# Optimization experiments

Hardware: AMD Instinct MI355X
Metric: run time of the kernel (lower is better)

Reference implementation:

```python
import jax, jax.numpy as jnp
import numpy as np

V, D, T, L, H = 32000, 1024, 2048, 2, 16
HS = D // H  # per-head dim (head_size // nheads)
FF = 4 * D
EPS = 1e-5


def _ln(x, g, b):
    m = jnp.mean(x, axis=-1, keepdims=True)
    v = jnp.mean((x - m) ** 2, axis=-1, keepdims=True)
    return (x - m) * jax.lax.rsqrt(v + EPS) * g + b


def setup_inputs() -> dict:
    key = jax.random.key(0)
    ks = jax.random.split(key, 16)
    s = lambda k, shape, fan: jax.random.normal(k, shape, jnp.float32) * (fan ** -0.5)
    return {
        "inputs": jax.random.randint(ks[0], (1, T), 0, V, dtype=jnp.int64),
        "tok_emb": s(ks[1], (V, D), D),
        "pos_emb": s(ks[2], (T, D), D),
        "ln1_g": jnp.ones((L, D)), "ln1_b": jnp.zeros((L, D)),
        "wq": s(ks[3], (L, H, D, HS), D),
        "wk": s(ks[4], (L, H, D, HS), D),
        "wv": s(ks[5], (L, H, D, HS), D),
        "ln2_g": jnp.ones((L, D)), "ln2_b": jnp.zeros((L, D)),
        "w1": s(ks[6], (L, D, FF), D), "b1": jnp.zeros((L, FF)),
        "w2": s(ks[7], (L, FF, D), FF), "b2": jnp.zeros((L, D)),
        "lnf_g": jnp.ones((D,)), "lnf_b": jnp.zeros((D,)),
        "w_un": s(ks[8], (D, V), D), "b_un": jnp.zeros((V,)),
    }


def reference(inputs, tok_emb, pos_emb, ln1_g, ln1_b, wq, wk, wv,
              ln2_g, ln2_b, w1, b1, w2, b2, lnf_g, lnf_b, w_un, b_un):
    b, t = inputs.shape
    x = tok_emb[inputs] + pos_emb[:t]  # [B,T,D]
    mask = jnp.tril(jnp.ones((t, t), dtype=bool))
    scale = jnp.asarray(D, x.dtype) ** -0.5  # source scales by x.shape[-1]**-0.5
    neg_inf = jnp.asarray(-jnp.inf, x.dtype)
    for l in range(L):
        h = _ln(x, ln1_g[l], ln1_b[l])
        q = jnp.einsum('btc,hcs->bhts', h, wq[l])
        k = jnp.einsum('btc,hcs->bhts', h, wk[l])
        v = jnp.einsum('btc,hcs->bhts', h, wv[l])
        scores = jnp.einsum('bhts,bhus->bhtu', q, k) * scale  # [B,H,T,T]
        scores = jnp.where(mask, scores, neg_inf)
        p = jax.nn.softmax(scores, axis=-1)
        att = jnp.einsum('bhtu,bhus->bhts', p, v)  # [B,H,T,HS]
        att = att.transpose(0, 2, 1, 3).reshape(b, t, H * HS)
        x = x + att
        h = _ln(x, ln2_g[l], ln2_b[l])
        h = jax.nn.relu(h @ w1[l] + b1[l]) @ w2[l] + b2[l]
        x = x + h
    x = _ln(x, lnf_g, lnf_b)
    return x @ w_un + b_un  # [B,T,V]
```

## Files before the change

kernel.cpp:

```cpp
#include <hip/hip_runtime.h>
#include <hip/hip_bf16.h>

#define TT 2048
#define DD 1024
#define NH 16
#define HSZ 64
#define FFD 4096
#define VV 32000
#define NL 2

typedef __bf16 bf16x8 __attribute__((ext_vector_type(8)));
typedef float f32x4 __attribute__((ext_vector_type(4)));

__device__ __forceinline__ unsigned short f2bf(float f) {
    unsigned int u = __float_as_uint(f);
    return (unsigned short)((u + 0x7FFFu + ((u >> 16) & 1u)) >> 16);
}

#define GLL(gsrc, ldst) \
  __builtin_amdgcn_global_load_lds((const __attribute__((address_space(1))) void*)(gsrc), \
                                   (__attribute__((address_space(3))) void*)(ldst), 16, 0, 0)

#define SWZ64(L)  ((L) ^ ((((L) >> 7) & 3) << 4))
#define SWZ128(L) ((L) ^ ((((L) >> 7) & 7) << 4))

#define VMW(n) asm volatile("s_waitcnt vmcnt(" #n ")" ::: "memory")

__global__ __launch_bounds__(256) void embed_kernel(
    const int* __restrict__ idx, const float* __restrict__ tok,
    const float* __restrict__ pos, float* __restrict__ x)
{
    int t = blockIdx.x;
    int d4 = threadIdx.x * 4;
    int token = idx[t];
    float4 a = *(const float4*)&tok[(size_t)token * DD + d4];
    float4 p = *(const float4*)&pos[(size_t)t * DD + d4];
    float4 r;
    r.x = a.x + p.x; r.y = a.y + p.y; r.z = a.z + p.z; r.w = a.w + p.w;
    *(float4*)&x[(size_t)t * DD + d4] = r;
}

__global__ __launch_bounds__(256) void ln_kernel(
    const float* __restrict__ x, const float* __restrict__ g,
    const float* __restrict__ b, unsigned short* __restrict__ out)
{
    int t = blockIdx.x;
    int tid = threadIdx.x;
    int d4 = tid * 4;
    float4 xv = *(const float4*)&x[(size_t)t * DD + d4];
    float s  = xv.x + xv.y + xv.z + xv.w;
    float s2 = xv.x*xv.x + xv.y*xv.y + xv.z*xv.z + xv.w*xv.w;
    #pragma unroll
    for (int off = 32; off >= 1; off >>= 1) {
        s  += __shfl_xor(s,  off);
        s2 += __shfl_xor(s2, off);
    }
    __shared__ float ls[4], ls2[4];
    int w = tid >> 6;
    if ((tid & 63) == 0) { ls[w] = s; ls2[w] = s2; }
    __syncthreads();
    float sum  = ls[0] + ls[1] + ls[2] + ls[3];
    float sum2 = ls2[0] + ls2[1] + ls2[2] + ls2[3];
    float mean = sum * (1.0f / DD);
    float var  = sum2 * (1.0f / DD) - mean * mean;
    float r = rsqrtf(var + 1e-5f);
    float4 gv = *(const float4*)&g[d4];
    float4 bv = *(const float4*)&b[d4];
    ushort4 pk;
    pk.x = f2bf((xv.x - mean) * r * gv.x + bv.x);
    pk.y = f2bf((xv.y - mean) * r * gv.y + bv.y);
    pk.z = f2bf((xv.z - mean) * r * gv.z + bv.z);
    pk.w = f2bf((xv.w - mean) * r * gv.w + bv.w);
    *(ushort4*)&out[(size_t)t * DD + d4] = pk;
}

__global__ __launch_bounds__(256) void tcast(
    const float* __restrict__ src, unsigned short* __restrict__ dst,
    int R, int C, size_t sstride, size_t dstride)
{
    __shared__ float tile[64][65];
    const float* s = src + (size_t)blockIdx.z * sstride;
    unsigned short* d = dst + (size_t)blockIdx.z * dstride;
    int c0 = blockIdx.x * 64, r0 = blockIdx.y * 64;
    #pragma unroll
    for (int i = 0; i < 16; ++i) {
        int id = i * 256 + threadIdx.x;
        int rr = id >> 6, cc = id & 63;
        tile[rr][cc] = s[(size_t)(r0 + rr) * C + (c0 + cc)];
    }
    __syncthreads();
    #pragma unroll
    for (int i = 0; i < 16; ++i) {
        int id = i * 256 + threadIdx.x;
        int cc = id >> 6, rr = id & 63;
        d[(size_t)(c0 + cc) * R + (r0 + rr)] = f2bf(tile[rr][cc]);
    }
}

__global__ __launch_bounds__(256) void qkv_tcast(
    const float* __restrict__ wq, const float* __restrict__ wk,
    const float* __restrict__ wv, unsigned short* __restrict__ dst)
{
    __shared__ float tile[64][65];
    int l = blockIdx.z;
    int mat = blockIdx.y >> 4, hh = blockIdx.y & 15;
    const float* s = (mat == 0) ? wq : (mat == 1) ? wk : wv;
    s += (((size_t)l * NH + hh) * DD) * HSZ;
    int r0 = blockIdx.x * 64;
    #pragma unroll
    for (int i = 0; i < 16; ++i) {
        int id = i * 256 + threadIdx.x;
        int rr = id >> 6, cc = id & 63;
        tile[rr][cc] = s[(size_t)(r0 + rr) * HSZ + cc];
    }
    __syncthreads();
    unsigned short* d = dst + (size_t)l * 3072 * DD + ((size_t)mat * DD + hh * HSZ) * DD;
    #pragma unroll
    for (int i = 0; i < 16; ++i) {
        int id = i * 256 + threadIdx.x;
        int cc = id >> 6, rr = id & 63;
        d[(size_t)cc * DD + (r0 + rr)] = f2bf(tile[rr][cc]);
    }
}

template<int EPI, int BN>
__global__ __launch_bounds__(256) void mgemm(
    const unsigned short* __restrict__ A, const unsigned short* __restrict__ Bt,
    const float* __restrict__ bias, void* __restrict__ outp,
    int M, int N, int K, int Kst)
{
    constexpr int FN = BN / 64 * 2;
    __shared__ unsigned short As[3][128 * 32];
    __shared__ unsigned short Bs[3][BN * 32];
    int tid = threadIdx.x;
    int w = tid >> 6, lane = tid & 63;
    int l15 = lane & 15, l4 = lane >> 4;
    int bm = blockIdx.y * 128, bn = blockIdx.x * BN;
    int wr = (w >> 1) * 64, wc = (w & 1) * (BN / 2);
    if (EPI == 3) {
        int z = blockIdx.z;
        A  += (size_t)z * K;
        Bt += (size_t)z * K;
        outp = (float*)outp + (size_t)z * TT * DD;
    }

    f32x4 zz = {0.f, 0.f, 0.f, 0.f};
    f32x4 acc[4][FN];
    #pragma unroll
    for (int m = 0; m < 4; ++m)
        #pragma unroll
        for (int n = 0; n < FN; ++n) acc[m][n] = zz;

    int t16 = tid * 16;
    int lg = SWZ64(t16);
    int srow = lg >> 6;
    int skel = (lg & 63) >> 1;
    const unsigned short* aS0 = A + (size_t)(bm + srow) * Kst + skel;
    const unsigned short* aS1 = A + (size_t)(bm + 64 + srow) * Kst + skel;
    const unsigned short* bS0 = Bt + (size_t)(bn + srow) * Kst + skel;
    const unsigned short* bS1 = Bt + (size_t)(bn + 64 + srow) * Kst + skel;

    #define STAGE(t, slot) do { int kk_ = (t) * 32; \
        GLL(aS0 + kk_, (char*)As[slot] + w * 1024); \
        GLL(aS1 + kk_, (char*)As[slot] + 4096 + w * 1024); \
        GLL(bS0 + kk_, (char*)Bs[slot] + w * 1024); \
        if (BN == 128) GLL(bS1 + kk_, (char*)Bs[slot] + 4096 + w * 1024); } while (0)

    int aoff[4], boff[FN];
    #pragma unroll
    for (int m = 0; m < 4; ++m)
        aoff[m] = SWZ64((wr + m * 16 + l15) * 64 + l4 * 16);
    #pragma unroll
    for (int n = 0; n < FN; ++n)
        boff[n] = SWZ64((wc + n * 16 + l15) * 64 + l4 * 16);

    int nt = K >> 5;
    STAGE(0, 0);
    STAGE(1, 1);
    STAGE(2, 2);
    int slot = 0;
    for (int t = 0; t < nt; ++t) {
        if (BN == 128) {
            if (t + 2 < nt)      VMW(8);
            else if (t + 1 < nt) VMW(4);
            else                 VMW(0);
        } else {
            if (t + 2 < nt)      VMW(6);
            else if (t + 1 < nt) VMW(3);
            else                 VMW(0);
        }
        __builtin_amdgcn_sched_barrier(0);
        __builtin_amdgcn_s_barrier();
        __builtin_amdgcn_sched_barrier(0);
        bf16x8 af[4], bfr[FN];
        #pragma unroll
        for (int m = 0; m < 4; ++m) af[m] = *(const bf16x8*)((const char*)As[slot] + aoff[m]);
        #pragma unroll
        for (int n = 0; n < FN; ++n) bfr[n] = *(const bf16x8*)((const char*)Bs[slot] + boff[n]);
        #pragma unroll
        for (int m = 0; m < 4; ++m)
            #pragma unroll
            for (int n = 0; n < FN; ++n)
                acc[m][n] = __builtin_amdgcn_mfma_f32_16x16x32_bf16(af[m], bfr[n], acc[m][n], 0, 0, 0);
        __builtin_amdgcn_sched_barrier(0);
        __builtin_amdgcn_s_barrier();
        __builtin_amdgcn_sched_barrier(0);
        if (t + 3 < nt) STAGE(t + 3, slot);
        slot = (slot == 2) ? 0 : slot + 1;
    }
    #undef STAGE

    #pragma unroll
    for (int m = 0; m < 4; ++m) {
        int row0 = bm + wr + m * 16 + l4 * 4;
        #pragma unroll
        for (int n = 0; n < FN; ++n) {
            int col = bn + wc + n * 16 + l15;
            f32x4 v = acc[m][n];
            if (EPI == 0) {
                int mat = col >> 10, hh = (col >> 6) & 15, ss = col & 63;
                unsigned short* base = (unsigned short*)outp + (size_t)mat * ((size_t)NH * TT * HSZ);
                if (mat < 2) {
                    #pragma unroll
                    for (int i = 0; i < 4; ++i)
                        base[((size_t)hh * TT + row0 + i) * HSZ + ss] = f2bf(v[i]);
                } else {
                    ushort4 pk;
                    pk.x = f2bf(v[0]); pk.y = f2bf(v[1]); pk.z = f2bf(v[2]); pk.w = f2bf(v[3]);
                    *(ushort4*)&base[((size_t)hh * HSZ + ss) * TT + row0] = pk;
                }
            } else if (EPI == 1) {
                float bb = bias[col];
                unsigned short* o = (unsigned short*)outp;
                #pragma unroll
                for (int i = 0; i < 4; ++i)
                    o[(size_t)(row0 + i) * FFD + col] = f2bf(fmaxf(v[i] + bb, 0.f));
            } else if (EPI == 2) {
                float bb = bias[col];
                float* xx = (float*)outp;
                #pragma unroll
                for (int i = 0; i < 4; ++i)
                    xx[(size_t)(row0 + i) * DD + col] += v[i] + bb;
            } else {
                float* xx = (float*)outp;
                #pragma unroll
                for (int i = 0; i < 4; ++i)
                    xx[(size_t)(row0 + i) * DD + col] = v[i];
            }
        }
    }
}

__global__ __launch_bounds__(256) void ffn2_reduce(
    const float* __restrict__ P, const float* __restrict__ b2,
    float* __restrict__ x)
{
    int t = blockIdx.x;
    int d4 = threadIdx.x * 4;
    size_t o = (size_t)t * DD + d4;
    float4 p0 = *(const float4*)&P[o];
    float4 p1 = *(const float4*)&P[o + (size_t)TT * DD];
    float4 bb = *(const float4*)&b2[d4];
    float4 xv = *(float4*)&x[o];
    xv.x += p0.x + p1.x + bb.x;
    xv.y += p0.y + p1.y + bb.y;
    xv.z += p0.z + p1.z + bb.z;
    xv.w += p0.w + p1.w + bb.w;
    *(float4*)&x[o] = xv;
}

__global__ __launch_bounds__(512, 2) void mgemm256(
    const unsigned short* __restrict__ A, const unsigned short* __restrict__ Bt,
    const float* __restrict__ bias, float* __restrict__ outp,
    int M, int N, int K)
{
    __shared__ unsigned short As[2][2][128 * 64];
    __shared__ unsigned short Bs[2][2][128 * 64];
    int tid = threadIdx.x;
    int w = tid >> 6, lane = tid & 63;
    int l15 = lane & 15, l4 = lane >> 4;
    int wr = w >> 2, wc = w & 3;
    int bid = blockIdx.x;
    int xcd = bid & 7, j = bid >> 3;
    int mt = j & 7, p = xcd * 16 + (j >> 3);
    if (p >= N / 256) return;
    int bm = mt * 256, bn = p * 256;

    f32x4 zz = {0.f, 0.f, 0.f, 0.f};
    f32x4 acc[8][4];
    #pragma unroll
    for (int m = 0; m < 8; ++m)
        #pragma unroll
        for (int n = 0; n < 4; ++n) acc[m][n] = zz;

    int L0 = w * 1024 + lane * 16;
    int Ls = SWZ128(L0);
    int srow = Ls >> 7;
    int skel = (Ls & 127) >> 1;
    const unsigned short* aS[2], *bS[2];
    aS[0] = A + (size_t)(bm + srow) * K + skel;
    aS[1] = A + (size_t)(bm + 128 + srow) * K + skel;
    bS[0] = Bt + (size_t)(bn + srow) * K + skel;
    bS[1] = Bt + (size_t)(bn + 128 + srow) * K + skel;
    size_t g1 = (size_t)64 * K;

    #define STAGE6(t, buf) do { int kk_ = (t) * 64; \
        GLL(aS[0] + kk_,      (char*)As[buf][0] + w * 1024); \
        GLL(aS[0] + g1 + kk_, (char*)As[buf][0] + 8192 + w * 1024); \
        GLL(aS[1] + kk_,      (char*)As[buf][1] + w * 1024); \
        GLL(aS[1] + g1 + kk_, (char*)As[buf][1] + 8192 + w * 1024); \
        GLL(bS[0] + kk_,      (char*)Bs[buf][0] + w * 1024); \
        GLL(bS[0] + g1 + kk_, (char*)Bs[buf][0] + 8192 + w * 1024); \
        GLL(bS[1] + kk_,      (char*)Bs[buf][1] + w * 1024); \
        GLL(bS[1] + g1 + kk_, (char*)Bs[buf][1] + 8192 + w * 1024); } while (0)

    int aoff[8][2], boff[4][2];
    #pragma unroll
    for (int m = 0; m < 8; ++m)
        #pragma unroll
        for (int ks = 0; ks < 2; ++ks) {
            int La = (m * 16 + l15) * 128 + ks * 64 + l4 * 16;
            aoff[m][ks] = SWZ128(La);
        }
    #pragma unroll
    for (int n = 0; n < 4; ++n)
        #pragma unroll
        for (int ks = 0; ks < 2; ++ks) {
            int Lb = ((wc & 1) * 64 + n * 16 + l15) * 128 + ks * 64 + l4 * 16;
            boff[n][ks] = SWZ128(Lb);
        }

    int nt = K >> 6;
    STAGE6(0, 0);
    STAGE6(1, 1);
    for (int t = 0; t < nt; ++t) {
        int buf = t & 1;
        if (t + 1 < nt) VMW(8);
        else            VMW(0);
        __builtin_amdgcn_sched_barrier(0);
        __builtin_amdgcn_s_barrier();
        __builtin_amdgcn_sched_barrier(0);
        const char* ab = (const char*)As[buf][wr];
        const char* bb = (const char*)Bs[buf][wc >> 1];
        bf16x8 bfr[4][2];
        #pragma unroll
        for (int n = 0; n < 4; ++n)
            #pragma unroll
            for (int ks = 0; ks < 2; ++ks)
                bfr[n][ks] = *(const bf16x8*)(bb + boff[n][ks]);
        __builtin_amdgcn_s_setprio(1);
        #pragma unroll
        for (int rh = 0; rh < 2; ++rh) {
            bf16x8 af[4][2];
            #pragma unroll
            for (int mm = 0; mm < 4; ++mm)
                #pragma unroll
                for (int ks = 0; ks < 2; ++ks)
                    af[mm][ks] = *(const bf16x8*)(ab + aoff[rh * 4 + mm][ks]);
            #pragma unroll
            for (int mm = 0; mm < 4; ++mm)
                #pragma unroll
                for (int n = 0; n < 4; ++n) {
                    acc[rh*4+mm][n] = __builtin_amdgcn_mfma_f32_16x16x32_bf16(af[mm][0], bfr[n][0], acc[rh*4+mm][n], 0, 0, 0);
                    acc[rh*4+mm][n] = __builtin_amdgcn_mfma_f32_16x16x32_bf16(af[mm][1], bfr[n][1], acc[rh*4+mm][n], 0, 0, 0);
                }
        }
        __builtin_amdgcn_s_setprio(0);
        __builtin_amdgcn_sched_barrier(0);
        __builtin_amdgcn_s_barrier();
        __builtin_amdgcn_sched_barrier(0);
        if (t + 2 < nt) STAGE6(t + 2, buf);
    }
    #undef STAGE6

    #pragma unroll
    for (int m = 0; m < 8; ++m) {
        int row0 = bm + wr * 128 + m * 16 + l4 * 4;
        #pragma unroll
        for (int n = 0; n < 4; ++n) {
            int col = bn + wc * 64 + n * 16 + l15;
            float bb = bias[col];
            f32x4 v = acc[m][n];
            #pragma unroll
            for (int i = 0; i < 4; ++i)
                outp[(size_t)(row0 + i) * VV + col] = v[i] + bb;
        }
    }
}

__global__ __launch_bounds__(256) void attn_kernel(
    const unsigned short* __restrict__ qg, const unsigned short* __restrict__ kg,
    const unsigned short* __restrict__ vt, float* __restrict__ x)
{
    __shared__ unsigned short Ks[2][64 * 64];
    __shared__ unsigned short Vs[2][64 * 64];
    __shared__ unsigned short Ps[4][16 * 64];
    int tid = threadIdx.x;
    int w = tid >> 6, lane = tid & 63;
    int l15 = lane & 15, l4 = lane >> 4;
    int hh = blockIdx.y;
    int qb = (31 - blockIdx.x) * 64;

    const unsigned short* qrow = qg + ((size_t)hh * TT + qb + w * 16 + l15) * HSZ + l4 * 8;
    bf16x8 qf0 = *(const bf16x8*)(qrow);
    bf16x8 qf1 = *(const bf16x8*)(qrow + 32);

    int t16 = tid * 16;
    int lgs = SWZ128(t16);
    int surow = lgs >> 7;
    int subyte = lgs & 127;
    const char* kbase = (const char*)(kg + (size_t)hh * TT * HSZ);
    const char* vbase = (const char*)(vt + (size_t)hh * HSZ * TT);

    #define ASTAGE(ib, buf) do { \
        int ub_ = (ib) * 64; \
        GLL(kbase + (size_t)(ub_ + surow) * 128 + subyte,          (char*)Ks[buf] + w * 1024); \
        GLL(kbase + (size_t)(ub_ + 32 + surow) * 128 + subyte,     (char*)Ks[buf] + 4096 + w * 1024); \
        GLL(vbase + (size_t)surow * 4096 + ub_ * 2 + subyte,       (char*)Vs[buf] + w * 1024); \
        GLL(vbase + (size_t)(surow + 32) * 4096 + ub_ * 2 + subyte,(char*)Vs[buf] + 4096 + w * 1024); \
    } while (0)

    f32x4 zz = {0.f, 0.f, 0.f, 0.f};
    f32x4 o[4];
    #pragma unroll
    for (int i = 0; i < 4; ++i) o[i] = zz;
    float mrun = -INFINITY, lrun = 0.f;

    const float scale = 0.03125f;
    int nkv = (qb >> 6) + 1;
    ASTAGE(0, 0);
    if (nkv > 1) ASTAGE(1, 1);
    int cur = 0;
    for (int ib = 0; ib < nkv; ++ib) {
        bool diag = (ib * 64 == qb);
        if (ib + 1 < nkv) VMW(4);
        else              VMW(0);
        __builtin_amdgcn_sched_barrier(0);
        __builtin_amdgcn_s_barrier();
        __builtin_amdgcn_sched_barrier(0);
        const char* ksc = (const char*)Ks[cur];
        const char* vsc = (const char*)Vs[cur];

        f32x4 sfr[4];
        __builtin_amdgcn_s_setprio(1);
        #pragma unroll
        for (int f = 0; f < 4; ++f) {
            int lgb = (f * 16 + l15) * 128 + l4 * 16;
            bf16x8 k0 = *(const bf16x8*)(ksc + SWZ128(lgb));
            bf16x8 k1 = *(const bf16x8*)(ksc + SWZ128(lgb + 64));
            f32x4 z = zz;
            z = __builtin_amdgcn_mfma_f32_16x16x32_bf16(k0, qf0, z, 0, 0, 0);
            z = __builtin_amdgcn_mfma_f32_16x16x32_bf16(k1, qf1, z, 0, 0, 0);
            sfr[f] = z;
        }
        __builtin_amdgcn_s_setprio(0);

        float mx = -INFINITY;
        #pragma unroll
        for (int f = 0; f < 4; ++f)
            #pragma unroll
            for (int i = 0; i < 4; ++i) {
                float s = sfr[f][i] * scale;
                if (diag && (16 * f + (l4 << 2) + i) > (w * 16 + l15)) s = -INFINITY;
                sfr[f][i] = s;
                mx = fmaxf(mx, s);
            }
        mx = fmaxf(mx, __shfl_xor(mx, 16));
        mx = fmaxf(mx, __shfl_xor(mx, 32));
        bool grow = __any(mx > mrun + 8.0f);
        float c = 1.0f;
        if (grow) {
            float mn = fmaxf(mrun, mx);
            c = __expf(mrun - mn);
            mrun = mn;
        }
        float ps = 0.f;
        #pragma unroll
        for (int f = 0; f < 4; ++f)
            #pragma unroll
            for (int i = 0; i < 4; ++i) {
                float p = __expf(sfr[f][i] - mrun);
                sfr[f][i] = p;
                ps += p;
            }
        ps += __shfl_xor(ps, 16);
        ps += __shfl_xor(ps, 32);
        lrun = lrun * c + ps;
        if (grow) {
            #pragma unroll
            for (int i = 0; i < 4; ++i) {
                float ci = __shfl(c, (lane & 48) + (l4 << 2) + i);
                #pragma unroll
                for (int sf = 0; sf < 4; ++sf) o[sf][i] *= ci;
            }
        }

        unsigned short* pw = Ps[w];
        #pragma unroll
        for (int f = 0; f < 4; ++f) {
            unsigned a0 = ((unsigned)f2bf(sfr[f][0])) | (((unsigned)f2bf(sfr[f][1])) << 16);
            unsigned a1 = ((unsigned)f2bf(sfr[f][2])) | (((unsigned)f2bf(sfr[f][3])) << 16);
            int byte0 = l15 * 128 + (16 * f + (l4 << 2)) * 2;
            *(unsigned*)((char*)pw + SWZ128(byte0)) = a0;
            *(unsigned*)((char*)pw + SWZ128(byte0 + 4)) = a1;
        }
        bf16x8 pa0 = *(const bf16x8*)((const char*)pw + SWZ128(l15 * 128 + l4 * 16));
        bf16x8 pa1 = *(const bf16x8*)((const char*)pw + SWZ128(l15 * 128 + 64 + l4 * 16));
        __builtin_amdgcn_s_setprio(1);
        #pragma unroll
        for (int sf = 0; sf < 4; ++sf) {
            int lgb = (sf * 16 + l15) * 128 + l4 * 16;
            bf16x8 v0 = *(const bf16x8*)(vsc + SWZ128(lgb));
            bf16x8 v1 = *(const bf16x8*)(vsc + SWZ128(lgb + 64));
            o[sf] = __builtin_amdgcn_mfma_f32_16x16x32_bf16(pa0, v0, o[sf], 0, 0, 0);
            o[sf] = __builtin_amdgcn_mfma_f32_16x16x32_bf16(pa1, v1, o[sf], 0, 0, 0);
        }
        __builtin_amdgcn_s_setprio(0);
        __builtin_amdgcn_sched_barrier(0);
        __builtin_amdgcn_s_barrier();
        __builtin_amdgcn_sched_barrier(0);
        if (ib + 2 < nkv) ASTAGE(ib + 2, cur);
        cur ^= 1;
    }
    #undef ASTAGE
    float rl[4];
    #pragma unroll
    for (int i = 0; i < 4; ++i)
        rl[i] = 1.0f / __shfl(lrun, (lane & 48) + (l4 << 2) + i);
    #pragma unroll
    for (int sf = 0; sf < 4; ++sf)
        #pragma unroll
        for (int i = 0; i < 4; ++i) {
            int q = qb + w * 16 + l4 * 4 + i;
            int d = hh * HSZ + sf * 16 + l15;
            x[(size_t)q * DD + d] += o[sf][i] * rl[i];
        }
}

extern "C" void kernel_launch(void* const* d_in, const int* in_sizes, int n_in,
                              void* d_out, int out_size, void* d_ws, size_t ws_size,
                              hipStream_t stream)
{
    const int*   idx    = (const int*)  d_in[0];
    const float* tok    = (const float*)d_in[1];
    const float* pos    = (const float*)d_in[2];
    const float* ln1_g  = (const float*)d_in[3];
    const float* ln1_b  = (const float*)d_in[4];
    const float* wq     = (const float*)d_in[5];
    const float* wk     = (const float*)d_in[6];
    const float* wv     = (const float*)d_in[7];
    const float* ln2_g  = (const float*)d_in[8];
    const float* ln2_b  = (const float*)d_in[9];
    const float* w1     = (const float*)d_in[10];
    const float* b1     = (const float*)d_in[11];
    const float* w2     = (const float*)d_in[12];
    const float* b2     = (const float*)d_in[13];
    const float* lnf_g  = (const float*)d_in[14];
    const float* lnf_b  = (const float*)d_in[15];
    const float* w_un   = (const float*)d_in[16];
    const float* b_un   = (const float*)d_in[17];
    float* out = (float*)d_out;

    char* W = (char*)d_ws;
    float*          x    = (float*)(W);
    unsigned short* h    = (unsigned short*)(W + 8388608);
    unsigned short* qg   = (unsigned short*)(W + 12582912);
    unsigned short* kg   = (unsigned short*)(W + 16777216);
    unsigned short* vt   = (unsigned short*)(W + 20971520);
    float*          Pp   = (float*)(W + 8388608);
    unsigned short* h1   = (unsigned short*)(W + 25165824);
    unsigned short* wqkvT= (unsigned short*)(W + 41943040);
    unsigned short* w1T  = (unsigned short*)(W + 54525952);
    unsigned short* w2T  = (unsigned short*)(W + 71303168);
    unsigned short* wunT = (unsigned short*)(W + 88080384);
    (void)kg; (void)ws_size; (void)in_sizes; (void)n_in; (void)out_size;

    qkv_tcast<<<dim3(16, 48, 2), 256, 0, stream>>>(wq, wk, wv, wqkvT);
    tcast<<<dim3(64, 16, 2), 256, 0, stream>>>(w1, w1T, DD, FFD, (size_t)DD * FFD, (size_t)DD * FFD);
    tcast<<<dim3(16, 64, 2), 256, 0, stream>>>(w2, w2T, FFD, DD, (size_t)FFD * DD, (size_t)FFD * DD);
    tcast<<<dim3(500, 16, 1), 256, 0, stream>>>(w_un, wunT, DD, VV, 0, 0);

    embed_kernel<<<TT, 256, 0, stream>>>(idx, tok, pos, x);

    for (int l = 0; l < NL; ++l) {
        ln_kernel<<<TT, 256, 0, stream>>>(x, ln1_g + l * DD, ln1_b + l * DD, h);
        mgemm<0, 64><<<dim3(48, 16), 256, 0, stream>>>(h, wqkvT + (size_t)l * 3072 * DD, nullptr, qg, TT, 3072, DD, DD);
        attn_kernel<<<dim3(32, 16), 256, 0, stream>>>(qg, kg, vt, x);
        ln_kernel<<<TT, 256, 0, stream>>>(x, ln2_g + l * DD, ln2_b + l * DD, h);
        mgemm<1, 128><<<dim3(32, 16), 256, 0, stream>>>(h, w1T + (size_t)l * FFD * DD, b1 + (size_t)l * FFD, h1, TT, FFD, DD, DD);
        mgemm<3, 64><<<dim3(16, 16, 2), 256, 0, stream>>>(h1, w2T + (size_t)l * DD * FFD, nullptr, Pp, TT, DD, FFD / 2, FFD);
        ffn2_reduce<<<TT, 256, 0, stream>>>(Pp, b2 + (size_t)l * DD, x);
    }

    ln_kernel<<<TT, 256, 0, stream>>>(x, lnf_g, lnf_b, h);
    mgemm256<<<dim3(1024), 512, 0, stream>>>(h, wunT, b_un, out, TT, VV, DD);
}
```

Baseline: 616.1 us.

## Fuse LayerNorm into embed and FFN2 reduce kernels, remap attention blocks by XCD

Embedding and the FFN2 partial-sum reduce now also compute the next LayerNorm (ln1 of the next layer, or the final LN) and write the bf16 normalized activations. This drops three separate ln_kernel launches and their re-reads of x. The attention grid becomes 1D, with a block-id remap that places pairs of heads on the same XCD, aiming at better K/V L2 locality. The cost is a bit more per-block work in the fused kernels.

```diff
diff --git a/kernel.cpp b/kernel.cpp
--- a/kernel.cpp
+++ b/kernel.cpp
@@ -26,18 +26,45 @@
 
 #define VMW(n) asm volatile("s_waitcnt vmcnt(" #n ")" ::: "memory")
 
-__global__ __launch_bounds__(256) void embed_kernel(
+__global__ __launch_bounds__(256) void embed_ln(
     const int* __restrict__ idx, const float* __restrict__ tok,
-    const float* __restrict__ pos, float* __restrict__ x)
+    const float* __restrict__ pos, const float* __restrict__ g,
+    const float* __restrict__ b, float* __restrict__ x,
+    unsigned short* __restrict__ h)
 {
     int t = blockIdx.x;
-    int d4 = threadIdx.x * 4;
+    int tid = threadIdx.x;
+    int d4 = tid * 4;
     int token = idx[t];
     float4 a = *(const float4*)&tok[(size_t)token * DD + d4];
     float4 p = *(const float4*)&pos[(size_t)t * DD + d4];
-    float4 r;
-    r.x = a.x + p.x; r.y = a.y + p.y; r.z = a.z + p.z; r.w = a.w + p.w;
-    *(float4*)&x[(size_t)t * DD + d4] = r;
+    float4 xv;
+    xv.x = a.x + p.x; xv.y = a.y + p.y; xv.z = a.z + p.z; xv.w = a.w + p.w;
+    *(float4*)&x[(size_t)t * DD + d4] = xv;
+    float s  = xv.x + xv.y + xv.z + xv.w;
+    float s2 = xv.x*xv.x + xv.y*xv.y + xv.z*xv.z + xv.w*xv.w;
+    #pragma unroll
+    for (int off = 32; off >= 1; off >>= 1) {
+        s  += __shfl_xor(s,  off);
+        s2 += __shfl_xor(s2, off);
+    }
+    __shared__ float ls[4], ls2[4];
+    int w = tid >> 6;
+    if ((tid & 63) == 0) { ls[w] = s; ls2[w] = s2; }
+    __syncthreads();
+    float sum  = ls[0] + ls[1] + ls[2] + ls[3];
+    float sum2 = ls2[0] + ls2[1] + ls2[2] + ls2[3];
+    float mean = sum * (1.0f / DD);
+    float var  = sum2 * (1.0f / DD) - mean * mean;
+    float r = rsqrtf(var + 1e-5f);
+    float4 gv = *(const float4*)&g[d4];
+    float4 bv = *(const float4*)&b[d4];
+    ushort4 pk;
+    pk.x = f2bf((xv.x - mean) * r * gv.x + bv.x);
+    pk.y = f2bf((xv.y - mean) * r * gv.y + bv.y);
+    pk.z = f2bf((xv.z - mean) * r * gv.z + bv.z);
+    pk.w = f2bf((xv.w - mean) * r * gv.w + bv.w);
+    *(ushort4*)&h[(size_t)t * DD + d4] = pk;
 }
 
 __global__ __launch_bounds__(256) void ln_kernel(
@@ -251,12 +278,14 @@
     }
 }
 
-__global__ __launch_bounds__(256) void ffn2_reduce(
+__global__ __launch_bounds__(256) void ffn2_reduce_ln(
     const float* __restrict__ P, const float* __restrict__ b2,
-    float* __restrict__ x)
+    float* __restrict__ x, const float* __restrict__ g,
+    const float* __restrict__ b, unsigned short* __restrict__ h)
 {
     int t = blockIdx.x;
-    int d4 = threadIdx.x * 4;
+    int tid = threadIdx.x;
+    int d4 = tid * 4;
     size_t o = (size_t)t * DD + d4;
     float4 p0 = *(const float4*)&P[o];
     float4 p1 = *(const float4*)&P[o + (size_t)TT * DD];
@@ -267,6 +296,30 @@
     xv.z += p0.z + p1.z + bb.z;
     xv.w += p0.w + p1.w + bb.w;
     *(float4*)&x[o] = xv;
+    float s  = xv.x + xv.y + xv.z + xv.w;
+    float s2 = xv.x*xv.x + xv.y*xv.y + xv.z*xv.z + xv.w*xv.w;
+    #pragma unroll
+    for (int off = 32; off >= 1; off >>= 1) {
+        s  += __shfl_xor(s,  off);
+        s2 += __shfl_xor(s2, off);
+    }
+    __shared__ float ls[4], ls2[4];
+    int w = tid >> 6;
+    if ((tid & 63) == 0) { ls[w] = s; ls2[w] = s2; }
+    __syncthreads();
+    float sum  = ls[0] + ls[1] + ls[2] + ls[3];
+    float sum2 = ls2[0] + ls2[1] + ls2[2] + ls2[3];
+    float mean = sum * (1.0f / DD);
+    float var  = sum2 * (1.0f / DD) - mean * mean;
+    float r = rsqrtf(var + 1e-5f);
+    float4 gv = *(const float4*)&g[d4];
+    float4 bv = *(const float4*)&b[d4];
+    ushort4 pk;
+    pk.x = f2bf((xv.x - mean) * r * gv.x + bv.x);
+    pk.y = f2bf((xv.y - mean) * r * gv.y + bv.y);
+    pk.z = f2bf((xv.z - mean) * r * gv.z + bv.z);
+    pk.w = f2bf((xv.w - mean) * r * gv.w + bv.w);
+    *(ushort4*)&h[o] = pk;
 }
 
 __global__ __launch_bounds__(512, 2) void mgemm256(
@@ -398,8 +451,10 @@
     int tid = threadIdx.x;
     int w = tid >> 6, lane = tid & 63;
     int l15 = lane & 15, l4 = lane >> 4;
-    int hh = blockIdx.y;
-    int qb = (31 - blockIdx.x) * 64;
+    int bid = blockIdx.x;
+    int j = bid >> 3;
+    int hh = (bid & 7) * 2 + (j & 1);
+    int qb = (31 - (j >> 1)) * 64;
 
     const unsigned short* qrow = qg + ((size_t)hh * TT + qb + w * 16 + l15) * HSZ + l4 * 8;
     bf16x8 qf0 = *(const bf16x8*)(qrow);
@@ -580,18 +635,18 @@
     tcast<<<dim3(16, 64, 2), 256, 0, stream>>>(w2, w2T, FFD, DD, (size_t)FFD * DD, (size_t)FFD * DD);
     tcast<<<dim3(500, 16, 1), 256, 0, stream>>>(w_un, wunT, DD, VV, 0, 0);
 
-    embed_kernel<<<TT, 256, 0, stream>>>(idx, tok, pos, x);
+    embed_ln<<<TT, 256, 0, stream>>>(idx, tok, pos, ln1_g, ln1_b, x, h);
 
     for (int l = 0; l < NL; ++l) {
-        ln_kernel<<<TT, 256, 0, stream>>>(x, ln1_g + l * DD, ln1_b + l * DD, h);
         mgemm<0, 64><<<dim3(48, 16), 256, 0, stream>>>(h, wqkvT + (size_t)l * 3072 * DD, nullptr, qg, TT, 3072, DD, DD);
-        attn_kernel<<<dim3(32, 16), 256, 0, stream>>>(qg, kg, vt, x);
+        attn_kernel<<<512, 256, 0, stream>>>(qg, kg, vt, x);
         ln_kernel<<<TT, 256, 0, stream>>>(x, ln2_g + l * DD, ln2_b + l * DD, h);
         mgemm<1, 128><<<dim3(32, 16), 256, 0, stream>>>(h, w1T + (size_t)l * FFD * DD, b1 + (size_t)l * FFD, h1, TT, FFD, DD, DD);
         mgemm<3, 64><<<dim3(16, 16, 2), 256, 0, stream>>>(h1, w2T + (size_t)l * DD * FFD, nullptr, Pp, TT, DD, FFD / 2, FFD);
-        ffn2_reduce<<<TT, 256, 0, stream>>>(Pp, b2 + (size_t)l * DD, x);
-    }
-
-    ln_kernel<<<TT, 256, 0, stream>>>(x, lnf_g, lnf_b, h);
+        const float* ng = (l + 1 < NL) ? (ln1_g + (l + 1) * DD) : lnf_g;
+        const float* nb = (l + 1 < NL) ? (ln1_b + (l + 1) * DD) : lnf_b;
+        ffn2_reduce_ln<<<TT, 256, 0, stream>>>(Pp, b2 + (size_t)l * DD, x, ng, nb, h);
+    }
+
     mgemm256<<<dim3(1024), 512, 0, stream>>>(h, wunT, b_un, out, TT, VV, DD);
 }
```

New measurement: 599.9 us. 1.03x faster.
